# Performance work log

Measured on AMD Instinct MI355X. Metric: run time of the kernel, lower is better.

Reference implementation:

```python
import jax, jax.numpy as jnp
import numpy as np
from jax import lax

B, L, HID, H, KS, C = 2, 4096, 1024, 4, 4, 64
DH = HID // H
EPS = 1e-5


def setup_inputs():
    key = jax.random.key(0)
    ks = jax.random.split(key, 10)
    s = 0.02
    return {
        "x": jax.random.normal(ks[0], (B, L, HID), jnp.float32),
        "Wq": jax.random.normal(ks[1], (HID, HID), jnp.float32) * s,
        "Wk": jax.random.normal(ks[2], (HID, HID), jnp.float32) * s,
        "Wv": jax.random.normal(ks[3], (HID, HID), jnp.float32) * s,
        "conv_q": jax.random.normal(ks[4], (HID, 1, KS), jnp.float32) * 0.3,
        "conv_k": jax.random.normal(ks[5], (HID, 1, KS), jnp.float32) * 0.3,
        "conv_v": jax.random.normal(ks[6], (HID, 1, KS), jnp.float32) * 0.3,
        "Wbeta": jax.random.normal(ks[7], (H, HID), jnp.float32) * s,
        "rms_w": jnp.ones((HID,), jnp.float32),
        "Wo": jax.random.normal(ks[8], (HID, HID), jnp.float32) * s,
    }


def _silu(x):
    return x * jax.nn.sigmoid(x)


def _conv_act(x, w):
    # depthwise causal conv1d: torch pads both sides by KS-1 then truncates to L,
    # which equals left-pad KS-1 + valid conv. Then SiLU (as in _calculate_conv).
    y = lax.conv_general_dilated(x.transpose(0, 2, 1), w, (1,), [(KS - 1, 0)],
                                 feature_group_count=HID,
                                 dimension_numbers=('NCH', 'OIH', 'NCH'))
    return _silu(y).transpose(0, 2, 1)


def _l2norm(x):
    # matches F.normalize(p=2, dim=-1) with eps=1e-12
    return x / jnp.maximum(jnp.linalg.norm(x, axis=-1, keepdims=True), 1e-12)


def _chunk_delta_rule(Q, K, V, beta):
    b, l, h, d = Q.shape
    n = (l + C - 1) // C
    pad = n * C - l
    if pad:
        padw = ((0, 0), (0, pad), (0, 0), (0, 0))
        Q, K, V, beta = (jnp.pad(a, padw) for a in (Q, K, V, beta))
    Q, K, V = (a.reshape(b, n, C, h, d) for a in (Q, K, V))
    beta = beta.reshape(b, n, C, h, 1)
    Kb, Vb = K * beta, V * beta
    # T is SUMMED over heads in the source (single shared T per chunk).
    T = -jnp.tril(jnp.einsum('bnihd,bnjhd->bnij', Kb, K), -1) + jnp.eye(C, dtype=Q.dtype)
    # forward-substitution UT transform: T[i,:i] += T[i,:] @ T[:, :i], sequentially in i
    def body(i, T):
        row = T[:, :, i, :]                                  # (b,n,C)
        prod = jnp.einsum('bnj,bnjc->bnc', row, T)
        new = jnp.where(jnp.arange(C) < i, row + prod, row)
        return T.at[:, :, i, :].set(new)
    T = lax.fori_loop(1, C, body, T)
    W = jnp.einsum('bnij,bnjhd->bnihd', T, Kb)
    U = jnp.einsum('bnij,bnjhd->bnihd', T, Vb)

    def step(S, inp):
        q_i, k_i, w_i, u0 = inp                              # each (b,C,h,d)
        # torch.einsum('bchd,bhdd->bchd', ., S) extracts diag(S) (repeated 'd')
        dS = jnp.einsum('bhdd->bhd', S)
        u_i = u0 - w_i * dS[:, None]
        o_inter = q_i * dS[:, None]
        # source: A_i = einsum('bchd,bchd->bc', q, k).tril()  (tril over batch/chunk dims!)
        A = jnp.tril(jnp.einsum('bchd,bchd->bc', q_i, k_i))
        o_intra = jnp.einsum('bc,bchd->bchd', A, u_i)
        S = S + jnp.einsum('bchd,bche->bhde', k_i, u_i)
        return S, o_inter + o_intra

    S0 = jnp.zeros((b, h, d, d), Q.dtype)
    mv = lambda a: jnp.moveaxis(a, 1, 0)                     # chunks to scan axis
    S, O = lax.scan(step, S0, (mv(Q), mv(K), mv(W), mv(U)))
    O = jnp.moveaxis(O, 0, 1).reshape(b, n * C, h, d)[:, :l]
    return O, S


def _forward(x, Wq, Wk, Wv, conv_q, conv_k, conv_v, Wbeta, rms_w, Wo):
    q = _conv_act(x @ Wq.T, conv_q).reshape(B, L, H, DH)
    k = _conv_act(x @ Wk.T, conv_k).reshape(B, L, H, DH)
    v = _conv_act(x @ Wv.T, conv_v).reshape(B, L, H, DH)
    q, k, v = _silu(q), _silu(k), _silu(v)                   # second SiLU, as in source
    q, k = _l2norm(q), _l2norm(k)
    beta = jax.nn.sigmoid(x @ Wbeta.T)[..., None]            # (B,L,H,1)
    o, S = _chunk_delta_rule(q, k, v, beta)
    o = o.reshape(B, L, HID)
    o = o * lax.rsqrt(jnp.mean(o * o, axis=-1, keepdims=True) + EPS) * rms_w
    return o @ Wo.T, S


def reference(x, Wq, Wk, Wv, conv_q, conv_k, conv_v, Wbeta, rms_w, Wo):
    return _forward(x, Wq, Wk, Wv, conv_q, conv_k, conv_v, Wbeta, rms_w, Wo)
```

## Files before the change

kernel.cpp:

```cpp
#include <hip/hip_runtime.h>
#include <hip/hip_bf16.h>

#define L_SEQ 4096
#define HID 1024
#define NH 4
#define DH 256
#define CK 64
#define BL_TOT 8192

typedef short v8s __attribute__((ext_vector_type(8)));
typedef unsigned short v8u __attribute__((ext_vector_type(8)));
typedef unsigned short v4us __attribute__((ext_vector_type(4)));
typedef float v4f __attribute__((ext_vector_type(4)));

typedef __attribute__((address_space(1))) const void* as1cv;
typedef __attribute__((address_space(3))) void* as3v;

__device__ __forceinline__ unsigned short f2bu(float f) {
    __hip_bfloat16 h = __float2bfloat16(f);
    return *(unsigned short*)&h;
}
__device__ __forceinline__ float bu2f(unsigned short u) {
    __hip_bfloat16 h = *(__hip_bfloat16*)&u;
    return __bfloat162float(h);
}

__global__ __launch_bounds__(256) void wcvt_kernel(const float* __restrict__ s0, const float* __restrict__ s1,
                                                   const float* __restrict__ s2, const float* __restrict__ s3,
                                                   unsigned short* __restrict__ d0, unsigned short* __restrict__ d1,
                                                   unsigned short* __restrict__ d2, unsigned short* __restrict__ d3) {
    const float* s = blockIdx.y == 0 ? s0 : blockIdx.y == 1 ? s1 : blockIdx.y == 2 ? s2 : s3;
    unsigned short* d = blockIdx.y == 0 ? d0 : blockIdx.y == 1 ? d1 : blockIdx.y == 2 ? d2 : d3;
    int i = blockIdx.x * 256 + threadIdx.x;
    int stride = gridDim.x * 256;
    for (; i < HID * HID; i += stride) d[i] = f2bu(s[i]);
}

__global__ __launch_bounds__(256) void gemm_mfma(const unsigned short* __restrict__ Ah,
                                                 const unsigned short* __restrict__ Bh,
                                                 float* __restrict__ C, int M, int N, int K) {
    __shared__ unsigned short AsH[128 * 32];
    __shared__ unsigned short BsH[128 * 32];
    const int tid = threadIdx.x;
    const int wave = tid >> 6, lane = tid & 63;
    const int quad = lane >> 4, l16 = lane & 15;
    const int m0 = blockIdx.x * 128, n0 = blockIdx.y * 128;
    const int wm = (wave >> 1) * 64, wn = (wave & 1) * 64;

    const int srow = wave * 16 + (lane >> 2);
    const int scol = (lane & 3) * 8;
    const unsigned short* Ag = Ah + (size_t)(m0 + srow) * K + scol;
    const unsigned short* Bg = Bh + (size_t)(n0 + srow) * K + scol;
    char* lA = (char*)AsH;
    char* lB = (char*)BsH;
    const int lbase = wave * 1024;

    v4f acc[4][4];
#pragma unroll
    for (int a = 0; a < 4; ++a)
#pragma unroll
        for (int b = 0; b < 4; ++b) { v4f z = {0.f, 0.f, 0.f, 0.f}; acc[a][b] = z; }

    for (int k0 = 0; k0 < K; k0 += 32) {
        __syncthreads();
        __builtin_amdgcn_global_load_lds((as1cv)(Ag + k0), (as3v)(lA + lbase), 16, 0, 0);
        __builtin_amdgcn_global_load_lds((as1cv)(Ag + (size_t)64 * K + k0), (as3v)(lA + 4096 + lbase), 16, 0, 0);
        __builtin_amdgcn_global_load_lds((as1cv)(Bg + k0), (as3v)(lB + lbase), 16, 0, 0);
        __builtin_amdgcn_global_load_lds((as1cv)(Bg + (size_t)64 * K + k0), (as3v)(lB + 4096 + lbase), 16, 0, 0);
        __syncthreads();
        v8s afh[4], bfh[4];
#pragma unroll
        for (int mt = 0; mt < 4; ++mt) afh[mt] = *(const v8s*)&AsH[(wm + mt * 16 + l16) * 32 + quad * 8];
#pragma unroll
        for (int nt = 0; nt < 4; ++nt) bfh[nt] = *(const v8s*)&BsH[(wn + nt * 16 + l16) * 32 + quad * 8];
#pragma unroll
        for (int mt = 0; mt < 4; ++mt)
#pragma unroll
            for (int nt = 0; nt < 4; ++nt)
                acc[mt][nt] = __builtin_amdgcn_mfma_f32_16x16x32_bf16(afh[mt], bfh[nt], acc[mt][nt], 0, 0, 0);
    }
#pragma unroll
    for (int mt = 0; mt < 4; ++mt)
#pragma unroll
        for (int nt = 0; nt < 4; ++nt) {
            int row = m0 + wm + mt * 16 + quad * 4;
            int col = n0 + wn + nt * 16 + l16;
#pragma unroll
            for (int r = 0; r < 4; ++r)
                C[(size_t)(row + r) * N + col] = acc[mt][nt][r];
        }
}

__global__ __launch_bounds__(256) void beta_kernel(const float* __restrict__ x,
                                                   const float* __restrict__ Wb,
                                                   float* __restrict__ betaB,
                                                   unsigned short* __restrict__ xh) {
    const int t = blockIdx.x;
    const int tid = threadIdx.x;
    const int wave = tid >> 6, lane = tid & 63;
    const float* xr = x + (size_t)t * HID;
    v4f xv = *(const v4f*)(xr + tid * 4);
    v4us xp;
#pragma unroll
    for (int i = 0; i < 4; ++i) xp[i] = f2bu(xv[i]);
    *(v4us*)&xh[(size_t)t * HID + tid * 4] = xp;
    float s[4];
#pragma unroll
    for (int h = 0; h < 4; ++h) {
        v4f wv = *(const v4f*)(Wb + (size_t)h * HID + tid * 4);
        s[h] = xv[0] * wv[0] + xv[1] * wv[1] + xv[2] * wv[2] + xv[3] * wv[3];
    }
#pragma unroll
    for (int off = 32; off; off >>= 1)
#pragma unroll
        for (int h = 0; h < 4; ++h) s[h] += __shfl_down(s[h], off);
    __shared__ float red[4][4];
    if (lane == 0)
#pragma unroll
        for (int h = 0; h < 4; ++h) red[wave][h] = s[h];
    __syncthreads();
    if (tid < 4) {
        float tot = red[0][tid] + red[1][tid] + red[2][tid] + red[3][tid];
        betaB[(size_t)t * 4 + tid] = 1.f / (1.f + expf(-tot));
    }
}

__global__ __launch_bounds__(256) void conv_kernel(const float* __restrict__ G, int gstride, int pathArg,
                                                   const float* __restrict__ wq, const float* __restrict__ wk,
                                                   const float* __restrict__ wv,
                                                   unsigned short* __restrict__ Vout,
                                                   unsigned short* __restrict__ KhiO, unsigned short* __restrict__ KloO,
                                                   unsigned short* __restrict__ Qout) {
    const int p = pathArg < 0 ? (int)blockIdx.y : pathArg;
    const int yoff = pathArg < 0 ? p * 1024 : 0;
    const float* __restrict__ w = p == 0 ? wv : p == 1 ? wk : wq;
    const int bl = blockIdx.x;
    const int l = bl & (L_SEQ - 1);
    const int tid = threadIdx.x;
    const int lane = tid & 63;
    const int c4 = (tid >> 6) * 256 + lane * 4;
    v4f wrow[4];
#pragma unroll
    for (int cc = 0; cc < 4; ++cc) wrow[cc] = *(const v4f*)&w[(c4 + cc) * 4];
    v4f acc = {0.f, 0.f, 0.f, 0.f};
#pragma unroll
    for (int j = 0; j < 4; ++j) {
        int ls = l - 3 + j;
        if (ls >= 0) {
            v4f g = *(const v4f*)&G[(size_t)(bl - 3 + j) * gstride + yoff + c4];
#pragma unroll
            for (int cc = 0; cc < 4; ++cc) acc[cc] += g[cc] * wrow[cc][j];
        }
    }
    float vals[4];
#pragma unroll
    for (int cc = 0; cc < 4; ++cc) {
        float a = acc[cc];
        float s1 = a / (1.f + expf(-a));
        vals[cc] = s1 / (1.f + expf(-s1));
    }
    if (p >= 1) {
        float sq = vals[0] * vals[0] + vals[1] * vals[1] + vals[2] * vals[2] + vals[3] * vals[3];
#pragma unroll
        for (int off = 32; off; off >>= 1) sq += __shfl_xor(sq, off);
        float nrm = 1.f / fmaxf(sqrtf(sq), 1e-12f);
#pragma unroll
        for (int cc = 0; cc < 4; ++cc) vals[cc] *= nrm;
    }
    const size_t ob = (size_t)bl * HID + c4;
    if (p == 1) {
        v4us hv, lv;
#pragma unroll
        for (int cc = 0; cc < 4; ++cc) {
            unsigned short h = f2bu(vals[cc]);
            hv[cc] = h;
            lv[cc] = f2bu(vals[cc] - bu2f(h));
        }
        *(v4us*)&KhiO[ob] = hv;
        *(v4us*)&KloO[ob] = lv;
    } else {
        unsigned short* O = p == 0 ? Vout : Qout;
        v4us hv;
#pragma unroll
        for (int cc = 0; cc < 4; ++cc) hv[cc] = f2bu(vals[cc]);
        *(v4us*)&O[ob] = hv;
    }
}

__global__ __launch_bounds__(256) void gram_kernel(const unsigned short* __restrict__ Khi,
                                                   const unsigned short* __restrict__ Klo,
                                                   float* __restrict__ Gg) {
    const int chunk = blockIdx.x;
    const int h = blockIdx.y;
    const int tid = threadIdx.x;
    const int wave = tid >> 6, lane = tid & 63;
    const int quad = lane >> 4, l16 = lane & 15;
    __shared__ unsigned short Hs[64 * 264];
    __shared__ unsigned short Ls[64 * 264];
    const int l0 = chunk * 64;
    const int cb = h * 256;
#pragma unroll
    for (int p = 0; p < 8; ++p) {
        int row = p * 8 + (tid >> 5);
        int col = (tid & 31) * 8;
        v8u hv = *(const v8u*)(Khi + (size_t)(l0 + row) * HID + cb + col);
        v8u lv = *(const v8u*)(Klo + (size_t)(l0 + row) * HID + cb + col);
        *(v8u*)&Hs[row * 264 + col] = hv;
        *(v8u*)&Ls[row * 264 + col] = lv;
    }
    __syncthreads();
    const int wm = wave * 16;
    v4f acc[4];
#pragma unroll
    for (int nt = 0; nt < 4; ++nt) { v4f z = {0.f, 0.f, 0.f, 0.f}; acc[nt] = z; }
#pragma unroll
    for (int ks = 0; ks < 8; ++ks) {
        v8s ah = *(const v8s*)&Hs[(wm + l16) * 264 + ks * 32 + quad * 8];
        v8s al = *(const v8s*)&Ls[(wm + l16) * 264 + ks * 32 + quad * 8];
#pragma unroll
        for (int nt = 0; nt < 4; ++nt) {
            v8s bh = *(const v8s*)&Hs[(nt * 16 + l16) * 264 + ks * 32 + quad * 8];
            v8s bl = *(const v8s*)&Ls[(nt * 16 + l16) * 264 + ks * 32 + quad * 8];
            acc[nt] = __builtin_amdgcn_mfma_f32_16x16x32_bf16(ah, bh, acc[nt], 0, 0, 0);
            acc[nt] = __builtin_amdgcn_mfma_f32_16x16x32_bf16(ah, bl, acc[nt], 0, 0, 0);
            acc[nt] = __builtin_amdgcn_mfma_f32_16x16x32_bf16(al, bh, acc[nt], 0, 0, 0);
        }
    }
    float* og = Gg + ((size_t)chunk * 4 + h) * 4096;
#pragma unroll
    for (int nt = 0; nt < 4; ++nt)
#pragma unroll
        for (int r = 0; r < 4; ++r)
            og[(wm + quad * 4 + r) * 64 + nt * 16 + l16] = acc[nt][r];
}

__global__ __launch_bounds__(256) void trec_kernel(const float* __restrict__ Gg,
                                                   const float* __restrict__ betaB,
                                                   float* __restrict__ Tg) {
    const int chunk = blockIdx.x;
    const int tid = threadIdx.x;
    const int wave = tid >> 6, lane = tid & 63;
    const int quad = lane >> 4, l16 = lane & 15;
    const int wm = wave * 16;
    __shared__ unsigned short BhR[64 * 72], BlR[64 * 72];
    __shared__ unsigned short BhT[64 * 72], BlT[64 * 72];
    __shared__ unsigned short PhR[64 * 72], PlR[64 * 72];
    __shared__ float Pf[64 * 73];
    __shared__ float betS[256];
    betS[tid] = betaB[(size_t)chunk * 256 + tid];
    __syncthreads();
    const float* gg = Gg + (size_t)chunk * 4 * 4096;
#pragma unroll
    for (int s = 0; s < 16; ++s) {
        int idx = tid + 256 * s;
        int i = idx >> 6, j = idx & 63;
        float a = 0.f;
        if (i > j) {
            a = -(betS[i * 4 + 0] * gg[idx] + betS[i * 4 + 1] * gg[4096 + idx] +
                  betS[i * 4 + 2] * gg[2 * 4096 + idx] + betS[i * 4 + 3] * gg[3 * 4096 + idx]);
        }
        unsigned short ah = f2bu(a);
        unsigned short al = f2bu(a - bu2f(ah));
        BhR[i * 72 + j] = ah;
        BlR[i * 72 + j] = al;
        BhT[j * 72 + i] = ah;
        BlT[j * 72 + i] = al;
        float p = (i == j) ? 1.f : 0.f;
        Pf[i * 73 + j] = p;
        PhR[i * 72 + j] = f2bu(p);
        PlR[i * 72 + j] = 0;
    }
    __syncthreads();

    for (int st = 0; st < 6; ++st) {
        v8s aBh[2], aBl[2], aPh[2], aPl[2];
        v8s bTh[2][4], bTl[2][4];
#pragma unroll
        for (int kk = 0; kk < 2; ++kk) {
            aBh[kk] = *(const v8s*)&BhR[(wm + l16) * 72 + kk * 32 + quad * 8];
            aBl[kk] = *(const v8s*)&BlR[(wm + l16) * 72 + kk * 32 + quad * 8];
            aPh[kk] = *(const v8s*)&PhR[(wm + l16) * 72 + kk * 32 + quad * 8];
            aPl[kk] = *(const v8s*)&PlR[(wm + l16) * 72 + kk * 32 + quad * 8];
#pragma unroll
            for (int nt = 0; nt < 4; ++nt) {
                bTh[kk][nt] = *(const v8s*)&BhT[(nt * 16 + l16) * 72 + kk * 32 + quad * 8];
                bTl[kk][nt] = *(const v8s*)&BlT[(nt * 16 + l16) * 72 + kk * 32 + quad * 8];
            }
        }
        v4f accP[4], accB[4];
#pragma unroll
        for (int nt = 0; nt < 4; ++nt) {
#pragma unroll
            for (int r = 0; r < 4; ++r)
                accP[nt][r] = Pf[(wm + quad * 4 + r) * 73 + nt * 16 + l16];
            v4f z = {0.f, 0.f, 0.f, 0.f};
            accB[nt] = z;
        }
        __syncthreads();
#pragma unroll
        for (int kk = 0; kk < 2; ++kk)
#pragma unroll
            for (int nt = 0; nt < 4; ++nt) {
                accP[nt] = __builtin_amdgcn_mfma_f32_16x16x32_bf16(aPh[kk], bTh[kk][nt], accP[nt], 0, 0, 0);
                accP[nt] = __builtin_amdgcn_mfma_f32_16x16x32_bf16(aPh[kk], bTl[kk][nt], accP[nt], 0, 0, 0);
                accP[nt] = __builtin_amdgcn_mfma_f32_16x16x32_bf16(aPl[kk], bTh[kk][nt], accP[nt], 0, 0, 0);
            }
        if (st < 5) {
#pragma unroll
            for (int kk = 0; kk < 2; ++kk)
#pragma unroll
                for (int nt = 0; nt < 4; ++nt) {
                    accB[nt] = __builtin_amdgcn_mfma_f32_16x16x32_bf16(aBh[kk], bTh[kk][nt], accB[nt], 0, 0, 0);
                    accB[nt] = __builtin_amdgcn_mfma_f32_16x16x32_bf16(aBh[kk], bTl[kk][nt], accB[nt], 0, 0, 0);
                    accB[nt] = __builtin_amdgcn_mfma_f32_16x16x32_bf16(aBl[kk], bTh[kk][nt], accB[nt], 0, 0, 0);
                }
        }
#pragma unroll
        for (int nt = 0; nt < 4; ++nt)
#pragma unroll
            for (int r = 0; r < 4; ++r) {
                int row = wm + quad * 4 + r;
                int col = nt * 16 + l16;
                float pv = accP[nt][r];
                Pf[row * 73 + col] = pv;
                unsigned short ph = f2bu(pv);
                PhR[row * 72 + col] = ph;
                PlR[row * 72 + col] = f2bu(pv - bu2f(ph));
                if (st < 5) {
                    float bv = accB[nt][r];
                    unsigned short bh2 = f2bu(bv);
                    unsigned short bl2 = f2bu(bv - bu2f(bh2));
                    BhR[row * 72 + col] = bh2;
                    BlR[row * 72 + col] = bl2;
                    BhT[col * 72 + row] = bh2;
                    BlT[col * 72 + row] = bl2;
                }
            }
        __syncthreads();
    }
#pragma unroll
    for (int s = 0; s < 16; ++s) {
        int idx = tid + 256 * s;
        int i = idx >> 6, j = idx & 63;
        float t = (i == j) ? 1.f : 3.f * Pf[i * 73 + j];
        Tg[(size_t)chunk * 4096 + idx] = t;
    }
}

__global__ __launch_bounds__(256) void wu_mfma_kernel(const float* __restrict__ Tg,
                                                      const unsigned short* __restrict__ Khi,
                                                      const unsigned short* __restrict__ Vhi,
                                                      const float* __restrict__ betaB,
                                                      unsigned short* __restrict__ Wb,
                                                      unsigned short* __restrict__ Ub,
                                                      float* __restrict__ kw, float* __restrict__ ku) {
    const int chunk = blockIdx.x;
    const int h = blockIdx.y;
    const int half = blockIdx.z;
    const int tid = threadIdx.x;
    const int wave = tid >> 6, lane = tid & 63;
    const int quad = lane >> 4, l16 = lane & 15;
    const size_t l0 = (size_t)chunk * 64;
    const int f0 = h * 256 + half * 128;
    __shared__ unsigned short Th[64 * 72], Tl[64 * 72];
    __shared__ unsigned short KT[128 * 72], VT[128 * 72];
    __shared__ float betS[64];
    if (tid < 64) betS[tid] = betaB[(l0 + tid) * 4 + h];
    __syncthreads();
#pragma unroll
    for (int s = 0; s < 16; ++s) {
        int idx = tid + 256 * s;
        int c = idx >> 6, j = idx & 63;
        float v = Tg[(size_t)chunk * 4096 + idx] * betS[j];
        unsigned short hv = f2bu(v);
        Th[c * 72 + j] = hv;
        Tl[c * 72 + j] = f2bu(v - bu2f(hv));
    }
#pragma unroll
    for (int pass = 0; pass < 4; ++pass) {
        int j = pass * 16 + (tid >> 4);
        int fc = (tid & 15) * 8;
        v8u kv = *(const v8u*)(Khi + (l0 + j) * HID + f0 + fc);
        v8u vv = *(const v8u*)(Vhi + (l0 + j) * HID + f0 + fc);
#pragma unroll
        for (int i = 0; i < 8; ++i) {
            KT[(fc + i) * 72 + j] = kv[i];
            VT[(fc + i) * 72 + j] = vv[i];
        }
    }
    __syncthreads();

    const int nf = wave * 32;
    const int bb = chunk >> 6, nn = chunk & 63;
    const size_t obase = (((size_t)bb * 4 + h) * 64 + nn) * 256 + half * 128;

#pragma unroll
    for (int phase = 0; phase < 2; ++phase) {
        const unsigned short* BT = phase ? VT : KT;
        v4f acc[4][2];
#pragma unroll
        for (int mt = 0; mt < 4; ++mt)
#pragma unroll
            for (int nt = 0; nt < 2; ++nt) { v4f z = {0.f, 0.f, 0.f, 0.f}; acc[mt][nt] = z; }
#pragma unroll
        for (int k0 = 0; k0 < 64; k0 += 32) {
            v8s ah[4], al[4], bf[2];
#pragma unroll
            for (int mt = 0; mt < 4; ++mt) {
                ah[mt] = *(const v8s*)&Th[(mt * 16 + l16) * 72 + k0 + quad * 8];
                al[mt] = *(const v8s*)&Tl[(mt * 16 + l16) * 72 + k0 + quad * 8];
            }
#pragma unroll
            for (int nt = 0; nt < 2; ++nt)
                bf[nt] = *(const v8s*)&BT[(nf + nt * 16 + l16) * 72 + k0 + quad * 8];
#pragma unroll
            for (int mt = 0; mt < 4; ++mt)
#pragma unroll
                for (int nt = 0; nt < 2; ++nt) {
                    acc[mt][nt] = __builtin_amdgcn_mfma_f32_16x16x32_bf16(ah[mt], bf[nt], acc[mt][nt], 0, 0, 0);
                    acc[mt][nt] = __builtin_amdgcn_mfma_f32_16x16x32_bf16(al[mt], bf[nt], acc[mt][nt], 0, 0, 0);
                }
        }
        unsigned short* Out = phase ? Ub : Wb;
        float* kk = phase ? ku : kw;
#pragma unroll
        for (int nt = 0; nt < 2; ++nt) {
            const int fl = nf + nt * 16 + l16;
            float dot = 0.f;
#pragma unroll
            for (int mt = 0; mt < 4; ++mt)
#pragma unroll
                for (int r = 0; r < 4; ++r) {
                    const int c = mt * 16 + quad * 4 + r;
                    float wv = acc[mt][nt][r];
                    Out[(l0 + c) * HID + f0 + fl] = f2bu(wv);
                    dot += bu2f(KT[fl * 72 + c]) * wv;
                }
            dot += __shfl_xor(dot, 16);
            dot += __shfl_xor(dot, 32);
            if (quad == 0) kk[obase + fl] = dot;
        }
    }
}

__global__ __launch_bounds__(256) void scan_kernel(const float* __restrict__ kw,
                                                   const float* __restrict__ ku,
                                                   float* __restrict__ dsA) {
    const int bh = blockIdx.x;
    const int e = threadIdx.x;
    float ds = 0.f;
    for (int n = 0; n < 64; ++n) {
        size_t idx = ((size_t)bh * 64 + n) * 256 + e;
        dsA[idx] = ds;
        ds = ds * (1.f - kw[idx]) + ku[idx];
    }
}

__device__ __forceinline__ float block_sum(float v, float* red) {
#pragma unroll
    for (int off = 32; off; off >>= 1) v += __shfl_down(v, off);
    const int wave = threadIdx.x >> 6;
    if ((threadIdx.x & 63) == 0) red[wave] = v;
    __syncthreads();
    float t = red[0] + red[1] + red[2] + red[3];
    __syncthreads();
    return t;
}

__global__ __launch_bounds__(256) void o_kernel(const unsigned short* __restrict__ Qb,
                                                const unsigned short* __restrict__ Khi,
                                                const unsigned short* __restrict__ Wb,
                                                const unsigned short* __restrict__ Ub,
                                                const float* __restrict__ dsA,
                                                const float* __restrict__ rmsw,
                                                unsigned short* __restrict__ ob,
                                                unsigned short* __restrict__ ub) {
    const int bl = blockIdx.x;
    const int b = bl >> 12, l = bl & (L_SEQ - 1);
    const int n = l >> 6, cpos = l & 63;
    const int tid = threadIdx.x;
    const int hh = tid >> 6, le = (tid & 63) * 4;
    const int c4 = hh * 256 + le;
    __shared__ float red[4];
    const size_t rowb = (size_t)bl * HID;
    v4f dsv = *(const v4f*)&dsA[(((size_t)b * 4 + hh) * 64 + n) * 256 + le];
    v4us qu = *(const v4us*)&Qb[rowb + c4];
    float qv[4];
#pragma unroll
    for (int i = 0; i < 4; ++i) qv[i] = bu2f(qu[i]);
    const bool doA = (cpos <= b);
    float Aval = 0.f;
    if (doA) {
        v4us kq = *(const v4us*)&Khi[rowb + c4];
        float s = 0.f;
#pragma unroll
        for (int i = 0; i < 4; ++i) s += qv[i] * bu2f(kq[i]);
        Aval = block_sum(s, red);
    }
    v4us uu = *(const v4us*)&Ub[rowb + c4];
    v4us wu4 = *(const v4us*)&Wb[rowb + c4];
    float ss = 0.f, ov[4];
    v4us up;
#pragma unroll
    for (int i = 0; i < 4; ++i) {
        float u = bu2f(uu[i]) - bu2f(wu4[i]) * dsv[i];
        up[i] = f2bu(u);
        float o = qv[i] * dsv[i];
        if (doA) o += Aval * u;
        ov[i] = o;
        ss += o * o;
    }
    *(v4us*)&ub[rowb + c4] = up;
    float tot = block_sum(ss, red);
    float scale = rsqrtf(tot * (1.f / 1024.f) + 1e-5f);
    v4f rw = *(const v4f*)&rmsw[c4];
    v4us op;
#pragma unroll
    for (int i = 0; i < 4; ++i) op[i] = f2bu(ov[i] * scale * rw[i]);
    *(v4us*)&ob[rowb + c4] = op;
}

#define SNS 8
__global__ __launch_bounds__(256) void s_mfma_kernel(const unsigned short* __restrict__ Khi,
                                                     const unsigned short* __restrict__ Ub,
                                                     float* __restrict__ Spart) {
    const int bh = blockIdx.x;
    const int b = bh >> 2, h = bh & 3;
    const int dt = blockIdx.y;
    const int et = blockIdx.z & 1;
    const int ns = blockIdx.z >> 1;
    const int tid = threadIdx.x;
    const int wave = tid >> 6, lane = tid & 63;
    const int quad = lane >> 4, l16 = lane & 15;
    const int wm = (wave >> 1) * 64, wn = (wave & 1) * 64;
    __shared__ unsigned short Kt[128 * 40];
    __shared__ unsigned short Ut[128 * 40];
    const int cc = tid >> 3;
    const int dcol = (tid & 7) * 16;
    const size_t rowbase = (size_t)b * 4096 + (size_t)ns * 512;
    const int ck = h * 256 + dt * 128;
    const int ce = h * 256 + et * 128;
    v4f acc[4][4];
#pragma unroll
    for (int a = 0; a < 4; ++a)
#pragma unroll
        for (int c2 = 0; c2 < 4; ++c2) { v4f z = {0.f, 0.f, 0.f, 0.f}; acc[a][c2] = z; }

    for (int kt = 0; kt < 16; ++kt) {
        size_t row = rowbase + kt * 32 + cc;
        v8u k0 = *(const v8u*)(Khi + row * HID + ck + dcol);
        v8u k1 = *(const v8u*)(Khi + row * HID + ck + dcol + 8);
        v8u u0 = *(const v8u*)(Ub + row * HID + ce + dcol);
        v8u u1 = *(const v8u*)(Ub + row * HID + ce + dcol + 8);
        __syncthreads();
#pragma unroll
        for (int j = 0; j < 8; ++j) {
            Kt[(dcol + j) * 40 + cc] = k0[j];
            Kt[(dcol + 8 + j) * 40 + cc] = k1[j];
            Ut[(dcol + j) * 40 + cc] = u0[j];
            Ut[(dcol + 8 + j) * 40 + cc] = u1[j];
        }
        __syncthreads();
        v8s af[4], bf[4];
#pragma unroll
        for (int mt = 0; mt < 4; ++mt) af[mt] = *(const v8s*)&Kt[(wm + mt * 16 + l16) * 40 + quad * 8];
#pragma unroll
        for (int nt = 0; nt < 4; ++nt) bf[nt] = *(const v8s*)&Ut[(wn + nt * 16 + l16) * 40 + quad * 8];
#pragma unroll
        for (int mt = 0; mt < 4; ++mt)
#pragma unroll
            for (int nt = 0; nt < 4; ++nt)
                acc[mt][nt] = __builtin_amdgcn_mfma_f32_16x16x32_bf16(af[mt], bf[nt], acc[mt][nt], 0, 0, 0);
    }
    float* out = Spart + (size_t)ns * (8 * 256 * 256);
#pragma unroll
    for (int mt = 0; mt < 4; ++mt)
#pragma unroll
        for (int nt = 0; nt < 4; ++nt) {
            int row = dt * 128 + wm + mt * 16 + quad * 4;
            int col = et * 128 + wn + nt * 16 + l16;
#pragma unroll
            for (int r = 0; r < 4; ++r)
                out[((size_t)bh * 256 + row + r) * 256 + col] = acc[mt][nt][r];
        }
}

__global__ __launch_bounds__(256) void sreduce_kernel(const float* __restrict__ Spart,
                                                      float* __restrict__ out) {
    int i = blockIdx.x * 256 + threadIdx.x;
    float s = 0.f;
#pragma unroll
    for (int ns = 0; ns < SNS; ++ns) s += Spart[(size_t)ns * (8 * 256 * 256) + i];
    out[i] = s;
}

extern "C" void kernel_launch(void* const* d_in, const int* in_sizes, int n_in,
                              void* d_out, int out_size, void* d_ws, size_t ws_size,
                              hipStream_t stream) {
    const float* x     = (const float*)d_in[0];
    const float* Wq    = (const float*)d_in[1];
    const float* Wk    = (const float*)d_in[2];
    const float* Wv    = (const float*)d_in[3];
    const float* convq = (const float*)d_in[4];
    const float* convk = (const float*)d_in[5];
    const float* convv = (const float*)d_in[6];
    const float* Wbeta = (const float*)d_in[7];
    const float* rmsw  = (const float*)d_in[8];
    const float* Wo    = (const float*)d_in[9];

    char* ws = (char*)d_ws;
    size_t off = 0;
    auto alloc = [&](size_t bytes) {
        char* p = ws + off;
        off += (bytes + 255) & ~(size_t)255;
        return (void*)p;
    };
    const size_t MM = (size_t)HID * HID;
    unsigned short* xhi   = (unsigned short*)alloc((size_t)BL_TOT * HID * 2);
    unsigned short* Khi   = (unsigned short*)alloc((size_t)BL_TOT * HID * 2);
    unsigned short* wbQKV = (unsigned short*)alloc(3 * MM * 2);
    unsigned short* wbO   = (unsigned short*)alloc(MM * 2);
    unsigned short* Vhi   = (unsigned short*)alloc((size_t)BL_TOT * HID * 2);
    unsigned short* Wb16  = (unsigned short*)alloc((size_t)BL_TOT * HID * 2);
    unsigned short* Ub16  = (unsigned short*)alloc((size_t)BL_TOT * HID * 2);
    float* Tg    = (float*)alloc((size_t)128 * 4096 * 4);
    float* betaB = (float*)alloc((size_t)BL_TOT * 4 * 4);
    float* kwB   = (float*)alloc((size_t)8 * 64 * 256 * 4);
    float* kuB   = (float*)alloc((size_t)8 * 64 * 256 * 4);
    float* dsA   = (float*)alloc((size_t)8 * 64 * 256 * 4);
    const size_t gt_big = (size_t)BL_TOT * 3 * HID * 4;
    const size_t gt_small = (size_t)BL_TOT * HID * 4;
    const bool big = (off + gt_big) <= ws_size;
    float* Gt = (float*)alloc(big ? gt_big : gt_small);

    unsigned short* Qm = xhi;
    unsigned short* ob = Qm;
    float* Spart = Gt;

    float* out0 = (float*)d_out;
    float* out1 = out0 + (size_t)BL_TOT * HID;
    unsigned short* Klo = (unsigned short*)out0;
    unsigned short* ubf = (unsigned short*)out0 + 8388608;
    float* Gg = out0 + (size_t)4400000;

    dim3 blk(256);
    dim3 ggrid(BL_TOT / 128, HID / 128);

    wcvt_kernel<<<dim3(256, 4), blk, 0, stream>>>(Wv, Wk, Wq, Wo, wbQKV, wbQKV + MM, wbQKV + 2 * MM, wbO);
    beta_kernel<<<BL_TOT, blk, 0, stream>>>(x, Wbeta, betaB, xhi);

    if (big) {
        gemm_mfma<<<dim3(BL_TOT / 128, 3 * HID / 128), blk, 0, stream>>>(xhi, wbQKV, Gt, BL_TOT, 3 * HID, HID);
        conv_kernel<<<dim3(BL_TOT, 3), blk, 0, stream>>>(Gt, 3 * HID, -1, convq, convk, convv,
                                                         Vhi, Khi, Klo, Qm);
        gram_kernel<<<dim3(128, 4), blk, 0, stream>>>(Khi, Klo, Gg);
        trec_kernel<<<128, blk, 0, stream>>>(Gg, betaB, Tg);
    } else {
        gemm_mfma<<<ggrid, blk, 0, stream>>>(xhi, wbQKV, Gt, BL_TOT, HID, HID);
        conv_kernel<<<dim3(BL_TOT, 1), blk, 0, stream>>>(Gt, HID, 0, convq, convk, convv, Vhi, Khi, Klo, Qm);
        gemm_mfma<<<ggrid, blk, 0, stream>>>(xhi, wbQKV + MM, Gt, BL_TOT, HID, HID);
        conv_kernel<<<dim3(BL_TOT, 1), blk, 0, stream>>>(Gt, HID, 1, convq, convk, convv, Vhi, Khi, Klo, Qm);
        gram_kernel<<<dim3(128, 4), blk, 0, stream>>>(Khi, Klo, Gg);
        trec_kernel<<<128, blk, 0, stream>>>(Gg, betaB, Tg);
        gemm_mfma<<<ggrid, blk, 0, stream>>>(xhi, wbQKV + 2 * MM, Gt, BL_TOT, HID, HID);
        conv_kernel<<<dim3(BL_TOT, 1), blk, 0, stream>>>(Gt, HID, 2, convq, convk, convv, Vhi, Khi, Klo, Qm);
    }

    wu_mfma_kernel<<<dim3(128, 4, 2), blk, 0, stream>>>(Tg, Khi, Vhi, betaB, Wb16, Ub16, kwB, kuB);
    scan_kernel<<<8, blk, 0, stream>>>(kwB, kuB, dsA);
    o_kernel<<<BL_TOT, blk, 0, stream>>>(Qm, Khi, Wb16, Ub16, dsA, rmsw, ob, ubf);
    s_mfma_kernel<<<dim3(8, 2, 2 * SNS), blk, 0, stream>>>(Khi, ubf, Spart);
    sreduce_kernel<<<2048, blk, 0, stream>>>(Spart, out1);

    gemm_mfma<<<ggrid, blk, 0, stream>>>(ob, wbO, out0, BL_TOT, HID, HID);
}
```

Measured before the change: 392.9 us.

## Store QKV projection output in bf16 and swizzle GEMM LDS layout

Makes the GEMM output type a template parameter, so the fused QKV projection writes bf16 instead of fp32 and the conv kernel reads bf16. This halves the intermediate traffic for the projection. It also XOR-swizzles the column offset in the GEMM's LDS staging and fragment loads to reduce bank conflicts. In exchange it rounds the pre-conv activations to bf16, and it resizes the workspace so the reused Spart buffer still fits.

Measured after the change: 369.9 us. 1.06x faster.

```diff
diff --git a/kernel.cpp b/kernel.cpp
--- a/kernel.cpp
+++ b/kernel.cpp
@@ -24,6 +24,8 @@
     __hip_bfloat16 h = *(__hip_bfloat16*)&u;
     return __bfloat162float(h);
 }
+__device__ __forceinline__ void storec(float* p, float v) { *p = v; }
+__device__ __forceinline__ void storec(unsigned short* p, float v) { *p = f2bu(v); }
 
 __global__ __launch_bounds__(256) void wcvt_kernel(const float* __restrict__ s0, const float* __restrict__ s1,
                                                    const float* __restrict__ s2, const float* __restrict__ s3,
@@ -36,9 +38,10 @@
     for (; i < HID * HID; i += stride) d[i] = f2bu(s[i]);
 }
 
+template <typename OT>
 __global__ __launch_bounds__(256) void gemm_mfma(const unsigned short* __restrict__ Ah,
                                                  const unsigned short* __restrict__ Bh,
-                                                 float* __restrict__ C, int M, int N, int K) {
+                                                 OT* __restrict__ C, int M, int N, int K) {
     __shared__ unsigned short AsH[128 * 32];
     __shared__ unsigned short BsH[128 * 32];
     const int tid = threadIdx.x;
@@ -48,12 +51,13 @@
     const int wm = (wave >> 1) * 64, wn = (wave & 1) * 64;
 
     const int srow = wave * 16 + (lane >> 2);
-    const int scol = (lane & 3) * 8;
+    const int scol = (((lane & 3) ^ ((srow >> 1) & 3)) * 8);
     const unsigned short* Ag = Ah + (size_t)(m0 + srow) * K + scol;
     const unsigned short* Bg = Bh + (size_t)(n0 + srow) * K + scol;
     char* lA = (char*)AsH;
     char* lB = (char*)BsH;
     const int lbase = wave * 1024;
+    const int qsw = (quad ^ ((l16 >> 1) & 3)) * 8;
 
     v4f acc[4][4];
 #pragma unroll
@@ -70,9 +74,9 @@
         __syncthreads();
         v8s afh[4], bfh[4];
 #pragma unroll
-        for (int mt = 0; mt < 4; ++mt) afh[mt] = *(const v8s*)&AsH[(wm + mt * 16 + l16) * 32 + quad * 8];
-#pragma unroll
-        for (int nt = 0; nt < 4; ++nt) bfh[nt] = *(const v8s*)&BsH[(wn + nt * 16 + l16) * 32 + quad * 8];
+        for (int mt = 0; mt < 4; ++mt) afh[mt] = *(const v8s*)&AsH[(wm + mt * 16 + l16) * 32 + qsw];
+#pragma unroll
+        for (int nt = 0; nt < 4; ++nt) bfh[nt] = *(const v8s*)&BsH[(wn + nt * 16 + l16) * 32 + qsw];
 #pragma unroll
         for (int mt = 0; mt < 4; ++mt)
 #pragma unroll
@@ -87,7 +91,7 @@
             int col = n0 + wn + nt * 16 + l16;
 #pragma unroll
             for (int r = 0; r < 4; ++r)
-                C[(size_t)(row + r) * N + col] = acc[mt][nt][r];
+                storec(&C[(size_t)(row + r) * N + col], acc[mt][nt][r]);
         }
 }
 
@@ -125,7 +129,7 @@
     }
 }
 
-__global__ __launch_bounds__(256) void conv_kernel(const float* __restrict__ G, int gstride, int pathArg,
+__global__ __launch_bounds__(256) void conv_kernel(const unsigned short* __restrict__ G, int gstride, int pathArg,
                                                    const float* __restrict__ wq, const float* __restrict__ wk,
                                                    const float* __restrict__ wv,
                                                    unsigned short* __restrict__ Vout,
@@ -147,9 +151,9 @@
     for (int j = 0; j < 4; ++j) {
         int ls = l - 3 + j;
         if (ls >= 0) {
-            v4f g = *(const v4f*)&G[(size_t)(bl - 3 + j) * gstride + yoff + c4];
-#pragma unroll
-            for (int cc = 0; cc < 4; ++cc) acc[cc] += g[cc] * wrow[cc][j];
+            v4us g = *(const v4us*)&G[(size_t)(bl - 3 + j) * gstride + yoff + c4];
+#pragma unroll
+            for (int cc = 0; cc < 4; ++cc) acc[cc] += bu2f(g[cc]) * wrow[cc][j];
         }
     }
     float vals[4];
@@ -628,14 +632,16 @@
     float* kwB   = (float*)alloc((size_t)8 * 64 * 256 * 4);
     float* kuB   = (float*)alloc((size_t)8 * 64 * 256 * 4);
     float* dsA   = (float*)alloc((size_t)8 * 64 * 256 * 4);
-    const size_t gt_big = (size_t)BL_TOT * 3 * HID * 4;
-    const size_t gt_small = (size_t)BL_TOT * HID * 4;
-    const bool big = (off + gt_big) <= ws_size;
-    float* Gt = (float*)alloc(big ? gt_big : gt_small);
+    const size_t gt_big = (size_t)BL_TOT * 3 * HID * 2;
+    const size_t gt_small = (size_t)BL_TOT * HID * 2;
+    const size_t spart_bytes = (size_t)SNS * 8 * 256 * 256 * 4;
+    const bool big = (off + (gt_big > spart_bytes ? gt_big : spart_bytes)) <= ws_size;
+    unsigned short* Gt = (unsigned short*)alloc(big ? (gt_big > spart_bytes ? gt_big : spart_bytes)
+                                                    : (gt_small > spart_bytes ? gt_small : spart_bytes));
 
     unsigned short* Qm = xhi;
     unsigned short* ob = Qm;
-    float* Spart = Gt;
+    float* Spart = (float*)Gt;
 
     float* out0 = (float*)d_out;
     float* out1 = out0 + (size_t)BL_TOT * HID;
@@ -650,19 +656,20 @@
     beta_kernel<<<BL_TOT, blk, 0, stream>>>(x, Wbeta, betaB, xhi);
 
     if (big) {
-        gemm_mfma<<<dim3(BL_TOT / 128, 3 * HID / 128), blk, 0, stream>>>(xhi, wbQKV, Gt, BL_TOT, 3 * HID, HID);
+        gemm_mfma<unsigned short><<<dim3(BL_TOT / 128, 3 * HID / 128), blk, 0, stream>>>(
+            xhi, wbQKV, Gt, BL_TOT, 3 * HID, HID);
         conv_kernel<<<dim3(BL_TOT, 3), blk, 0, stream>>>(Gt, 3 * HID, -1, convq, convk, convv,
                                                          Vhi, Khi, Klo, Qm);
         gram_kernel<<<dim3(128, 4), blk, 0, stream>>>(Khi, Klo, Gg);
         trec_kernel<<<128, blk, 0, stream>>>(Gg, betaB, Tg);
     } else {
-        gemm_mfma<<<ggrid, blk, 0, stream>>>(xhi, wbQKV, Gt, BL_TOT, HID, HID);
+        gemm_mfma<unsigned short><<<ggrid, blk, 0, stream>>>(xhi, wbQKV, Gt, BL_TOT, HID, HID);
         conv_kernel<<<dim3(BL_TOT, 1), blk, 0, stream>>>(Gt, HID, 0, convq, convk, convv, Vhi, Khi, Klo, Qm);
-        gemm_mfma<<<ggrid, blk, 0, stream>>>(xhi, wbQKV + MM, Gt, BL_TOT, HID, HID);
+        gemm_mfma<unsigned short><<<ggrid, blk, 0, stream>>>(xhi, wbQKV + MM, Gt, BL_TOT, HID, HID);
         conv_kernel<<<dim3(BL_TOT, 1), blk, 0, stream>>>(Gt, HID, 1, convq, convk, convv, Vhi, Khi, Klo, Qm);
         gram_kernel<<<dim3(128, 4), blk, 0, stream>>>(Khi, Klo, Gg);
         trec_kernel<<<128, blk, 0, stream>>>(Gg, betaB, Tg);
-        gemm_mfma<<<ggrid, blk, 0, stream>>>(xhi, wbQKV + 2 * MM, Gt, BL_TOT, HID, HID);
+        gemm_mfma<unsigned short><<<ggrid, blk, 0, stream>>>(xhi, wbQKV + 2 * MM, Gt, BL_TOT, HID, HID);
         conv_kernel<<<dim3(BL_TOT, 1), blk, 0, stream>>>(Gt, HID, 2, convq, convk, convv, Vhi, Khi, Klo, Qm);
     }
 
@@ -672,5 +679,5 @@
     s_mfma_kernel<<<dim3(8, 2, 2 * SNS), blk, 0, stream>>>(Khi, ubf, Spart);
     sreduce_kernel<<<2048, blk, 0, stream>>>(Spart, out1);
 
-    gemm_mfma<<<ggrid, blk, 0, stream>>>(ob, wbO, out0, BL_TOT, HID, HID);
-}
+    gemm_mfma<float><<<ggrid, blk, 0, stream>>>(ob, wbO, out0, BL_TOT, HID, HID);
+}
```
